# Kernel optimization log

Measured on AMD Instinct MI355X. Metric: run time of the kernel, lower is better.

Reference implementation:

```python
import jax, jax.numpy as jnp
import numpy as np
from jax import lax

# QKeras quantized_bits(8, 0, alpha=1, keep_negative=1):
#   delta = 2^-(bits-1) = 1/128, q(x) = clip(round(x*128), -128, 127)/128
QB_SCALE = 128.0
# QKeras quantized_relu(8, 0): q(x) = clip(round(x*256), 0, 255)/256
QR_SCALE = 256.0

def _ste(q, x):
    # straight-through estimator: forward = q(x), backward = identity
    return x + lax.stop_gradient(q - x)

def qbits(x):
    q = jnp.clip(jnp.round(x * QB_SCALE), -QB_SCALE, QB_SCALE - 1.0) / QB_SCALE
    return _ste(q, x)

def qrelu(x):
    q = jnp.clip(jnp.round(x * QR_SCALE), 0.0, QR_SCALE - 1.0) / QR_SCALE
    return _ste(q, x)


def setup_inputs() -> dict:
    key = jax.random.key(0)
    ks = jax.random.split(key, 9)
    B, C, F = 1000000, 16, 3
    dims = [C * F, 64, 32, 32]
    x = jax.random.normal(ks[0], (B, C, F), dtype=jnp.float32)
    def w(k, i, o):
        return jax.random.normal(k, (i, o), dtype=jnp.float32) * (0.5 / np.sqrt(i))
    inp = {"x": x}
    for li in range(3):
        inp[f"w{li+1}"] = w(ks[1 + 2 * li], dims[li], dims[li + 1])
        inp[f"b{li+1}"] = jax.random.normal(ks[2 + 2 * li], (dims[li + 1],), dtype=jnp.float32) * 0.05
    inp["wout"] = w(ks[7], dims[-1], 5)
    inp["bout"] = jax.random.normal(ks[8], (5,), dtype=jnp.float32) * 0.05
    return inp


def reference(x, w1, b1, w2, b2, w3, b3, wout, bout):
    h = x.reshape(x.shape[0], -1)  # Flatten: [B, 48]
    for w, b in ((w1, b1), (w2, b2), (w3, b3)):
        # QDense: fake-quantize kernel & bias, fp32 matmul, quantized_relu
        h = qrelu(h @ qbits(w) + qbits(b))
    return h @ wout + bout  # final float Dense -> logits [B, 5]
```

## Files before the change

### kernel.cpp

```cpp
#include <hip/hip_runtime.h>
#include <hip/hip_bf16.h>

typedef short  short8 __attribute__((ext_vector_type(8)));
typedef float  f32x4  __attribute__((ext_vector_type(4)));
typedef unsigned int u32;
typedef unsigned long long u64;
typedef unsigned short u16;

__device__ __forceinline__ u32 f2bf(float v) {
    u32 u = __float_as_uint(v);
    return (u + 0x7FFFu + ((u >> 16) & 1u)) >> 16;
}
__device__ __forceinline__ float qround128(float w) {
    float q = rintf(w * 128.0f);
    return fminf(fmaxf(q, -128.0f), 127.0f);
}
__device__ __forceinline__ u32 cvtpk(float a, float b) {
    __hip_bfloat162 h = __float22bfloat162_rn(make_float2(a, b));
    union { __hip_bfloat162 h; u32 u; } cv; cv.h = h; return cv.u;
}
__device__ __forceinline__ float q255(float v) {
    return fminf(fmaxf(rintf(v), 0.f), 255.f);
}
union FragU { short8 s; u32 u[4]; };
__device__ __forceinline__ short8 pack2(f32x4 a, f32x4 b) {
    FragU f;
    f.u[0] = cvtpk(q255(a[0]), q255(a[1]));
    f.u[1] = cvtpk(q255(a[2]), q255(a[3]));
    f.u[2] = cvtpk(q255(b[0]), q255(b[1]));
    f.u[3] = cvtpk(q255(b[2]), q255(b[3]));
    return f.s;
}
__device__ __forceinline__ f32x4 mfma16(short8 a, short8 b, f32x4 c) {
    return __builtin_amdgcn_mfma_f32_16x16x32_bf16(a, b, c, 0, 0, 0);
}
__device__ __forceinline__ void gload16(const float* src, float* lds_dst) {
    __builtin_amdgcn_global_load_lds(
        (const __attribute__((address_space(1))) u32*)src,
        (__attribute__((address_space(3))) u32*)lds_dst,
        16, 0, 0);
}

__global__ void prep(const float* __restrict__ w1, const float* __restrict__ b1,
                     const float* __restrict__ w2, const float* __restrict__ b2,
                     const float* __restrict__ w3, const float* __restrict__ b3,
                     const float* __restrict__ wo, const float* __restrict__ bo,
                     u16* __restrict__ wsh) {
    int idx = blockIdx.x * 256 + threadIdx.x;
    if (idx < 16 * 512) {
        int blk = idx >> 9, e = idx & 511;
        int l = e >> 3, j = e & 7;
        int r  = l & 15;
        int gi = l >> 4;
        int fp = 16 * (j >> 2) + 4 * gi + (j & 3);
        float val = 0.f;
        if (blk < 8) {
            int mt = blk >> 1, ks = blk & 1;
            int fo = mt * 16 + r;
            if (ks == 0) {
                val = 2.0f * qround128(w1[(12 * gi + j) * 64 + fo]);
            } else if (j < 4) {
                val = 2.0f * qround128(w1[(12 * gi + 8 + j) * 64 + fo]);
            } else if (gi == 3 && j == 7) {
                val = 2.0f * qround128(b1[fo]);
            }
        } else if (blk < 12) {
            int bi = blk - 8, mt = bi >> 1, ks = bi & 1;
            int f = ks * 32 + fp, fo = mt * 16 + r;
            val = qround128(w2[f * 32 + fo]) * (1.0f / 128.0f);
        } else if (blk < 14) {
            int mt = blk - 12;
            val = qround128(w3[fp * 32 + mt * 16 + r]) * (1.0f / 128.0f);
        } else {
            float wv = (r < 5) ? wo[fp * 5 + r] * (1.0f / 256.0f) : 0.f;
            u32 hb = f2bf(wv);
            if (blk == 14) { wsh[idx] = (u16)hb; return; }
            val = wv - __uint_as_float(hb << 16);
        }
        wsh[idx] = (u16)f2bf(val);
    }
    if (blockIdx.x == 0) {
        int t = threadIdx.x;
        float* wsf = (float*)(wsh + 8192);
        for (int i = t; i < 32; i += 256) wsf[64 + i]  = 2.0f * qround128(b2[i]);
        for (int i = t; i < 32; i += 256) wsf[96 + i]  = 2.0f * qround128(b3[i]);
        for (int i = t; i < 16; i += 256) wsf[128 + i] = (i < 5) ? bo[i] : 0.f;
    }
}


__global__ __launch_bounds__(256, 3) void mlp_mfma(const float* __restrict__ x,
                                                   const u16* __restrict__ wsh,
                                                   float* __restrict__ out, int ntiles) {
    __shared__ __align__(16) float smem[4][2][1536];
    const int tid = threadIdx.x;
    const int wid = tid >> 6, lane = tid & 63;
    const int c = lane & 15, g = lane >> 4;

    short8 wf[16];
    const short8* wv = (const short8*)wsh;
    #pragma unroll
    for (int i = 0; i < 16; ++i) wf[i] = wv[i * 64 + lane];

    const float* wsf = (const float*)(wsh + 8192);
    f32x4 b2q[2], b3q[2], boq;
    #pragma unroll
    for (int i = 0; i < 2; ++i) b2q[i] = *(const f32x4*)(wsf + 64 + i * 16 + 4 * g);
    #pragma unroll
    for (int i = 0; i < 2; ++i) b3q[i] = *(const f32x4*)(wsf + 96 + i * 16 + 4 * g);
    boq = *(const f32x4*)(wsf + 128 + 4 * g);

    const int npacks = (ntiles + 1) >> 1;
    const int gw = blockIdx.x * 4 + wid;
    const int nw = gridDim.x * 4;
    const f32x4 zero4 = {0.f, 0.f, 0.f, 0.f};
    const int roff = c * 48 + g * 12;

    auto stage = [&](int buf, int pk) {
        #pragma unroll
        for (int s = 0; s < 6; ++s) {
            int tt = 2 * pk + (s >= 3 ? 1 : 0);
            if (tt >= ntiles) tt = ntiles - 1;
            const float* src = x + (size_t)tt * 768 + (s % 3) * 256 + lane * 4;
            gload16(src, &smem[wid][buf][s * 256]);
        }
    };

    int p = gw;
    int buf = 0;
    if (p < npacks) stage(0, p);

    for (; p < npacks; p += nw) {
        const int pn = p + nw;
        const bool have = pn < npacks;
        if (have) {
            stage(buf ^ 1, pn);
            asm volatile("s_waitcnt vmcnt(6)" ::: "memory");
        } else {
            asm volatile("s_waitcnt vmcnt(0)" ::: "memory");
        }
        __builtin_amdgcn_sched_barrier(0);

        #pragma unroll
        for (int i = 0; i < 2; ++i) {
            const float* T = &smem[wid][buf][i * 768];
            float4 q0 = *(const float4*)(T + roff);
            float4 q1 = *(const float4*)(T + roff + 4);
            float4 q2 = *(const float4*)(T + roff + 8);
            float v[12] = {q0.x, q0.y, q0.z, q0.w,
                           q1.x, q1.y, q1.z, q1.w,
                           q2.x, q2.y, q2.z, q2.w};

            FragU bh0, bl0, bh1, bl1;
            #pragma unroll
            for (int q = 0; q < 4; ++q) {
                u32 uu = cvtpk(v[2 * q], v[2 * q + 1]);
                bh0.u[q] = uu;
                float r0 = v[2 * q]     - __uint_as_float(uu << 16);
                float r1 = v[2 * q + 1] - __uint_as_float(uu & 0xFFFF0000u);
                bl0.u[q] = cvtpk(r0, r1);
            }
            #pragma unroll
            for (int q = 0; q < 2; ++q) {
                u32 uu = cvtpk(v[8 + 2 * q], v[9 + 2 * q]);
                bh1.u[q] = uu;
                float r0 = v[8 + 2 * q] - __uint_as_float(uu << 16);
                float r1 = v[9 + 2 * q] - __uint_as_float(uu & 0xFFFF0000u);
                bl1.u[q] = cvtpk(r0, r1);
            }
            bh1.u[2] = 0u;
            bh1.u[3] = (g == 3) ? 0x3F800000u : 0u;
            bl1.u[2] = 0u; bl1.u[3] = 0u;

            f32x4 acc1[4];
            #pragma unroll
            for (int mt = 0; mt < 4; ++mt) {
                f32x4 ah = mfma16(wf[mt * 2 + 0], bh0.s, zero4);
                ah = mfma16(wf[mt * 2 + 1], bh1.s, ah);
                f32x4 al = mfma16(wf[mt * 2 + 0], bl0.s, zero4);
                al = mfma16(wf[mt * 2 + 1], bl1.s, al);
                acc1[mt] = ah + al;
            }
            short8 p0 = pack2(acc1[0], acc1[1]);
            short8 p1 = pack2(acc1[2], acc1[3]);

            f32x4 a20 = mfma16(wf[8],  p0, b2q[0]);
            f32x4 a21 = mfma16(wf[9],  p1, zero4);
            f32x4 a22 = mfma16(wf[10], p0, b2q[1]);
            f32x4 a23 = mfma16(wf[11], p1, zero4);
            short8 p2 = pack2(a20 + a21, a22 + a23);

            f32x4 a30 = mfma16(wf[12], p2, b3q[0]);
            f32x4 a31 = mfma16(wf[13], p2, b3q[1]);
            short8 p3 = pack2(a30, a31);

            f32x4 aoh = mfma16(wf[14], p3, boq);
            f32x4 aol = mfma16(wf[15], p3, zero4);
            f32x4 ao = aoh + aol;

            int t = 2 * p + i;
            if (t < ntiles) {
                float* orow = out + (size_t)t * 80 + c * 5;
                if (g == 0) {
                    *(float4*)orow = make_float4(ao[0], ao[1], ao[2], ao[3]);
                } else if (g == 1) {
                    orow[4] = ao[0];
                }
            }
        }
        buf ^= 1;
    }
}

extern "C" void kernel_launch(void* const* d_in, const int* in_sizes, int n_in,
                              void* d_out, int out_size, void* d_ws, size_t ws_size,
                              hipStream_t stream) {
    const float* x  = (const float*)d_in[0];
    const float* w1 = (const float*)d_in[1];
    const float* b1 = (const float*)d_in[2];
    const float* w2 = (const float*)d_in[3];
    const float* b2 = (const float*)d_in[4];
    const float* w3 = (const float*)d_in[5];
    const float* b3 = (const float*)d_in[6];
    const float* wo = (const float*)d_in[7];
    const float* bo = (const float*)d_in[8];
    float* out = (float*)d_out;

    int B = in_sizes[0] / 48;
    int ntiles = B / 16;
    int npacks = (ntiles + 1) / 2;

    prep<<<32, 256, 0, stream>>>(w1, b1, w2, b2, w3, b3, wo, bo, (u16*)d_ws);

    int blocks = (npacks + 3) / 4;
    if (blocks > 2048) blocks = 2048;
    mlp_mfma<<<blocks, 256, 0, stream>>>(x, (const u16*)d_ws, out, ntiles);
}
```

Measured before the change: 51.40 us.

## Stage three tiles per pack with swizzled LDS layout and fixed grid

Each wave now stages three 16-row tiles per pack instead of two, with per-lane global-load offsets permuted so each lane later reads its 12 contiguous floats straight from LDS at lane*12 without a strided layout. The grid is fixed at 512 blocks, launch bounds drop to 2 waves per SIMD, and the wait count rises to 9 outstanding loads. The aim is more bytes in flight per wave and fewer LDS bank conflicts on the read side. In exchange the LDS footprint per block grows and occupancy is lower, and the scattered global-load addresses may coalesce less well.

```diff
diff --git a/kernel.cpp b/kernel.cpp
--- a/kernel.cpp
+++ b/kernel.cpp
@@ -89,10 +89,10 @@
 }
 
 
-__global__ __launch_bounds__(256, 3) void mlp_mfma(const float* __restrict__ x,
+__global__ __launch_bounds__(256, 2) void mlp_mfma(const float* __restrict__ x,
                                                    const u16* __restrict__ wsh,
                                                    float* __restrict__ out, int ntiles) {
-    __shared__ __align__(16) float smem[4][2][1536];
+    __shared__ __align__(16) float smem[4][2][3][768];
     const int tid = threadIdx.x;
     const int wid = tid >> 6, lane = tid & 63;
     const int c = lane & 15, g = lane >> 4;
@@ -110,19 +110,29 @@
     for (int i = 0; i < 2; ++i) b3q[i] = *(const f32x4*)(wsf + 96 + i * 16 + 4 * g);
     boq = *(const f32x4*)(wsf + 128 + 4 * g);
 
-    const int npacks = (ntiles + 1) >> 1;
+    u32 soff[3];
+    #pragma unroll
+    for (int s = 0; s < 3; ++s) {
+        int k = 64 * s + lane;
+        int l = k / 3, j = k - 3 * l;
+        soff[s] = (u32)((l & 15) * 48 + (l >> 4) * 12 + 4 * j);
+    }
+
+    const int npacks = (ntiles + 2) / 3;
     const int gw = blockIdx.x * 4 + wid;
     const int nw = gridDim.x * 4;
     const f32x4 zero4 = {0.f, 0.f, 0.f, 0.f};
-    const int roff = c * 48 + g * 12;
 
     auto stage = [&](int buf, int pk) {
         #pragma unroll
-        for (int s = 0; s < 6; ++s) {
-            int tt = 2 * pk + (s >= 3 ? 1 : 0);
+        for (int i = 0; i < 3; ++i) {
+            int tt = 3 * pk + i;
             if (tt >= ntiles) tt = ntiles - 1;
-            const float* src = x + (size_t)tt * 768 + (s % 3) * 256 + lane * 4;
-            gload16(src, &smem[wid][buf][s * 256]);
+            const float* tb = x + (size_t)tt * 768;
+            #pragma unroll
+            for (int s = 0; s < 3; ++s) {
+                gload16(tb + soff[s], &smem[wid][buf][i][s * 256]);
+            }
         }
     };
 
@@ -135,18 +145,18 @@
         const bool have = pn < npacks;
         if (have) {
             stage(buf ^ 1, pn);
-            asm volatile("s_waitcnt vmcnt(6)" ::: "memory");
+            asm volatile("s_waitcnt vmcnt(9)" ::: "memory");
         } else {
             asm volatile("s_waitcnt vmcnt(0)" ::: "memory");
         }
         __builtin_amdgcn_sched_barrier(0);
 
         #pragma unroll
-        for (int i = 0; i < 2; ++i) {
-            const float* T = &smem[wid][buf][i * 768];
-            float4 q0 = *(const float4*)(T + roff);
-            float4 q1 = *(const float4*)(T + roff + 4);
-            float4 q2 = *(const float4*)(T + roff + 8);
+        for (int i = 0; i < 3; ++i) {
+            const float* T = &smem[wid][buf][i][0] + lane * 12;
+            float4 q0 = *(const float4*)(T);
+            float4 q1 = *(const float4*)(T + 4);
+            float4 q2 = *(const float4*)(T + 8);
             float v[12] = {q0.x, q0.y, q0.z, q0.w,
                            q1.x, q1.y, q1.z, q1.w,
                            q2.x, q2.y, q2.z, q2.w};
@@ -198,7 +208,7 @@
             f32x4 aol = mfma16(wf[15], p3, zero4);
             f32x4 ao = aoh + aol;
 
-            int t = 2 * p + i;
+            int t = 3 * p + i;
             if (t < ntiles) {
                 float* orow = out + (size_t)t * 80 + c * 5;
                 if (g == 0) {
@@ -228,11 +238,9 @@
 
     int B = in_sizes[0] / 48;
     int ntiles = B / 16;
-    int npacks = (ntiles + 1) / 2;
 
     prep<<<32, 256, 0, stream>>>(w1, b1, w2, b2, w3, b3, wo, bo, (u16*)d_ws);
 
-    int blocks = (npacks + 3) / 4;
-    if (blocks > 2048) blocks = 2048;
+    int blocks = 512;
     mlp_mfma<<<blocks, 256, 0, stream>>>(x, (const u16*)d_ws, out, ntiles);
 }
```

Result: slower. 55.42 us (+7.8%).
